# Performance work log

Measured on AMD Instinct MI355X. Metric: run time of the kernel, lower is better.

Reference implementation:

```python
import jax, jax.numpy as jnp
import numpy as np

NC = 80
NA = 3
BOX_GAIN, CLS_GAIN, OBJ_GAIN = 7.5, 0.5, 1.0
GAMMA = 1.5
LS = 0.0
EPS = 1e-7
ANCHORS = np.array([[[10, 13], [16, 30], [33, 23]],
                    [[30, 61], [62, 45], [59, 119]],
                    [[116, 90], [156, 198], [373, 326]]], dtype=np.float32)


def bce_logits(x, t):
    # numerically stable BCE-with-logits, elementwise
    return jnp.maximum(x, 0.0) - x * t + jnp.log1p(jnp.exp(-jnp.abs(x)))


def iou_cxcywh(b1, b2, eps=EPS):
    b1x1, b1x2 = b1[..., 0] - b1[..., 2] / 2, b1[..., 0] + b1[..., 2] / 2
    b1y1, b1y2 = b1[..., 1] - b1[..., 3] / 2, b1[..., 1] + b1[..., 3] / 2
    b2x1, b2x2 = b2[..., 0] - b2[..., 2] / 2, b2[..., 0] + b2[..., 2] / 2
    b2y1, b2y2 = b2[..., 1] - b2[..., 3] / 2, b2[..., 1] + b2[..., 3] / 2
    inter = jnp.clip(jnp.minimum(b1x2, b2x2) - jnp.maximum(b1x1, b2x1), 0.0) * \
            jnp.clip(jnp.minimum(b1y2, b2y2) - jnp.maximum(b1y1, b2y1), 0.0)
    w1, h1 = b1x2 - b1x1, b1y2 - b1y1 + eps
    w2, h2 = b2x2 - b2x1, b2y2 - b2y1 + eps
    union = w1 * h1 + w2 * h2 - inter + eps
    return inter / union


def _scale_loss(pred, targets, anchors):
    B, C, h, w = pred.shape
    p = pred.reshape(B, NA, NC + 5, h, w).transpose(0, 1, 3, 4, 2)  # [B,3,h,w,nc+5]
    pobj = p[..., 4]

    N = targets.shape[0]
    scale = jnp.array([w, h, w, h], dtype=pred.dtype)
    g = targets[:, 2:6] * scale  # grid-space cx,cy,w,h
    gx, gy = g[:, 0], g[:, 1]
    valid = (gx >= 0) & (gx < w) & (gy >= 0) & (gy < h)
    gi = jnp.clip(jnp.floor(gx).astype(jnp.int32), 0, w - 1)
    gj = jnp.clip(jnp.floor(gy).astype(jnp.int32), 0, h - 1)
    bidx = jnp.clip(targets[:, 0].astype(jnp.int32), 0, B - 1)
    cls = jnp.clip(targets[:, 1].astype(jnp.int32), 0, NC - 1)

    # each GT is assigned to all 3 anchors -> M = 3N rows
    rep = lambda v: jnp.repeat(v, NA, axis=0)
    bM, giM, gjM, clsM, maskM = rep(bidx), rep(gi), rep(gj), rep(cls), rep(valid)
    aiM = jnp.tile(jnp.arange(NA), N)
    anchM = anchors[aiM]                             # [M,2]
    txyM = rep(g[:, :2] - jnp.floor(g[:, :2]))       # cell-relative offsets
    twhM = rep(g[:, 2:4])
    mf = maskM.astype(pred.dtype)
    n_valid = mf.sum()

    # objectness target grid (duplicates collapse to 1 via max, like repeated set)
    tobj = jnp.zeros((B, NA, h, w), pred.dtype).at[bM, aiM, gjM, giM].max(mf)
    loss_obj = bce_logits(pobj, tobj).mean() * OBJ_GAIN

    ps = p[bM, aiM, gjM, giM]                        # [M, nc+5]
    ps_box, ps_cls = ps[:, :4], ps[:, 5:]

    # focal classification loss
    t = jax.nn.one_hot(clsM, NC, dtype=pred.dtype)
    if LS > 0:
        t = t * (1 - LS) + LS / NC
    ce = bce_logits(ps_cls, t)
    focal = (1.0 - jnp.exp(-ce)) ** GAMMA * ce       # [M, nc]
    row_sum = (focal * mf[:, None]).sum(-1)          # [M]
    loss_cls = jnp.where(n_valid > 0,
                         row_sum.sum() / (jnp.maximum(n_valid, 1.0) * NC),
                         0.0) * CLS_GAIN

    # per-class focal means (rows grouped by GT class)
    seg_ids = jnp.where(maskM, clsM, NC)
    seg_sum = jax.ops.segment_sum(row_sum, seg_ids, num_segments=NC + 1)[:NC]
    seg_cnt = jax.ops.segment_sum(mf, seg_ids, num_segments=NC + 1)[:NC]
    per_class = jnp.where(seg_cnt > 0,
                          seg_sum / (jnp.maximum(seg_cnt, 1.0) * NC),
                          0.0) * CLS_GAIN

    # box (IoU) loss
    pxy = jax.nn.sigmoid(ps_box[:, :2]) * 2.0 - 0.5
    pwh = (jax.nn.sigmoid(ps_box[:, 2:4]) * 2.0) ** 2 * anchM
    pbox = jnp.concatenate([pxy, pwh], axis=-1)
    tbox = jnp.concatenate([txyM, twhM], axis=-1)
    iou = iou_cxcywh(pbox, tbox)
    loss_box = jnp.where(n_valid > 0,
                         ((1.0 - iou) * mf).sum() / jnp.maximum(n_valid, 1.0),
                         0.0) * BOX_GAIN

    return loss_box, loss_cls, loss_obj, per_class


def setup_inputs() -> dict:
    key = jax.random.key(0)
    k0, k1, k2, kb, kc, kxy, kwh = jax.random.split(key, 7)
    B, N = 16, 800
    p0 = jax.random.normal(k0, (B, NA * (NC + 5), 80, 80), jnp.float32)
    p1 = jax.random.normal(k1, (B, NA * (NC + 5), 40, 40), jnp.float32)
    p2 = jax.random.normal(k2, (B, NA * (NC + 5), 20, 20), jnp.float32)
    bcol = jax.random.randint(kb, (N, 1), 0, B).astype(jnp.float32)
    ccol = jax.random.randint(kc, (N, 1), 0, NC).astype(jnp.float32)
    xy = jax.random.uniform(kxy, (N, 2), jnp.float32, 0.02, 0.98)
    wh = jax.random.uniform(kwh, (N, 2), jnp.float32, 0.02, 0.30)
    targets = jnp.concatenate([bcol, ccol, xy, wh], axis=1)  # [N,6]
    return {"p0": p0, "p1": p1, "p2": p2, "targets": targets}


def reference(p0, p1, p2, targets):
    anchors = jnp.asarray(ANCHORS)
    lb = lc = lo = 0.0
    pc = jnp.zeros((NC,), jnp.float32)
    for i, pred in enumerate((p0, p1, p2)):
        b, c, o, per_class = _scale_loss(pred, targets, anchors[i])
        lb, lc, lo = lb + b, lc + c, lo + o
        pc = pc + per_class
    total = lb + lc + lo
    # [loss, loss_box, loss_cls, loss_obj, per-class cls losses...]
    return jnp.concatenate([jnp.stack([total, lb, lc, lo]), pc])
```

## Files before the change

### kernel.cpp

```cpp
#include <hip/hip_runtime.h>
#include <math.h>

#define NC 80
#define TCOLS 6
#define RPB 15

__device__ __constant__ float c_anch[3][3][2] = {
  {{10.f,13.f},{16.f,30.f},{33.f,23.f}},
  {{30.f,61.f},{62.f,45.f},{59.f,119.f}},
  {{116.f,90.f},{156.f,198.f},{373.f,326.f}}
};

#define ACC_CORR   0
#define ACC_OBJ    16
#define ACC_BOX(s) (32 + 16*(s))
#define ACC_CLS(s) (80 + 16*(s))
#define ACC_NV(s)  (128 + 16*(s))
#define ACC_SEG    176
#define ACC_TOTAL  (176 + 6*NC)

__device__ __forceinline__ float fbce0(float x) {
  return fmaxf(x, 0.f) + __logf(1.f + __expf(-fabsf(x)));
}
__device__ __forceinline__ float fbce(float x, float t) {
  return fmaxf(x, 0.f) - x * t + __logf(1.f + __expf(-fabsf(x)));
}
__device__ __forceinline__ float ffocal(float x, float t) {
  float ce = fbce(x, t);
  float u  = 1.f - __expf(-ce);
  return u * __builtin_amdgcn_sqrtf(u) * ce;
}

__global__ void k_init(float* __restrict__ acc) {
  for (int k = threadIdx.x; k < ACC_TOTAL; k += 256) acc[k] = 0.f;
}

__global__ __launch_bounds__(1024, 8)
void k_fused(const float* __restrict__ p0, const float* __restrict__ p1,
             const float* __restrict__ p2, const float* __restrict__ tgt,
             int N, int B, int RB, int OBJB, float* __restrict__ acc) {
  const int bid = blockIdx.x;
  const int tid = threadIdx.x;
  __shared__ float red[16];

  if (bid < RB) {
    __shared__ float l_box[3], l_cls[3], l_nv[3];
    if (tid < 3) { l_box[tid]=0.f; l_cls[tid]=0.f; l_nv[tid]=0.f; }
    __syncthreads();
    int wv    = tid >> 6;
    int lane  = tid & 63;
    int row   = bid * RPB + wv;
    int nrows = 9 * N;
    if (wv < RPB && row < nrows) {
      int rps = N * 3;
      int s   = row / rps;
      int rem = row - s * rps;
      int n   = rem / 3;
      int a   = rem - n * 3;
      int w   = (s == 0) ? 80 : ((s == 1) ? 40 : 20);
      int hw  = w * w;
      const float* pred = (s == 0) ? p0 : ((s == 1) ? p1 : p2);
      float fw = (float)w;
      float gx = tgt[n*TCOLS + 2] * fw, gy = tgt[n*TCOLS + 3] * fw;
      if (gx >= 0.f && gx < fw && gy >= 0.f && gy < fw) {
        float gw = tgt[n*TCOLS + 4] * fw, gh = tgt[n*TCOLS + 5] * fw;
        int gi  = min(max((int)floorf(gx), 0), w - 1);
        int gj  = min(max((int)floorf(gy), 0), w - 1);
        int b   = min(max((int)tgt[n*TCOLS + 0], 0), B - 1);
        int cls = min(max((int)tgt[n*TCOLS + 1], 0), NC - 1);
        size_t base = (size_t)(b*255 + a*85) * hw + (size_t)(gj*w + gi);

        float x0  = pred[base + (size_t)(5 + lane) * hw];
        float x1  = (lane < 16) ? pred[base + (size_t)(69 + lane) * hw] : 0.f;
        float bxv = (lane < 4)  ? pred[base + (size_t)lane * hw] : 0.f;

        float rs = ffocal(x0, (lane == cls) ? 1.f : 0.f);
        if (lane < 16) rs += ffocal(x1, ((64 + lane) == cls) ? 1.f : 0.f);
        for (int off = 32; off > 0; off >>= 1) rs += __shfl_xor(rs, off, 64);

        float bx = __shfl(bxv, 0, 64), by = __shfl(bxv, 1, 64);
        float bw = __shfl(bxv, 2, 64), bh = __shfl(bxv, 3, 64);
        if (lane == 0) {
          float sx = 1.f/(1.f + __expf(-bx));
          float sy = 1.f/(1.f + __expf(-by));
          float sw = 1.f/(1.f + __expf(-bw));
          float sh = 1.f/(1.f + __expf(-bh));
          float px = sx*2.f - 0.5f, py = sy*2.f - 0.5f;
          float aw = c_anch[s][a][0], ah = c_anch[s][a][1];
          float pw = (sw*2.f)*(sw*2.f)*aw, ph = (sh*2.f)*(sh*2.f)*ah;
          float txf = gx - floorf(gx), tyf = gy - floorf(gy);
          float b1x1 = px - pw*0.5f, b1x2 = px + pw*0.5f;
          float b1y1 = py - ph*0.5f, b1y2 = py + ph*0.5f;
          float b2x1 = txf - gw*0.5f, b2x2 = txf + gw*0.5f;
          float b2y1 = tyf - gh*0.5f, b2y2 = tyf + gh*0.5f;
          float iw = fmaxf(fminf(b1x2, b2x2) - fmaxf(b1x1, b2x1), 0.f);
          float ih = fmaxf(fminf(b1y2, b2y2) - fmaxf(b1y1, b2y1), 0.f);
          float inter = iw * ih;
          float w1 = b1x2 - b1x1, h1 = b1y2 - b1y1 + 1e-7f;
          float w2 = b2x2 - b2x1, h2 = b2y2 - b2y1 + 1e-7f;
          float uni = w1*h1 + w2*h2 - inter + 1e-7f;
          float iou = inter / uni;

          atomicAdd(&l_box[s], 1.f - iou);
          atomicAdd(&l_cls[s], rs);
          atomicAdd(&l_nv[s],  1.f);
          atomicAdd(&acc[ACC_SEG +        s*NC + cls], rs);
          atomicAdd(&acc[ACC_SEG + 3*NC + s*NC + cls], 1.f);
        }
      }
    }
    __syncthreads();
    if (tid < 3) {
      int s = tid; float v;
      v = l_box[s]; if (v != 0.f) atomicAdd(&acc[ACC_BOX(s)], v);
      v = l_cls[s]; if (v != 0.f) atomicAdd(&acc[ACC_CLS(s)], v);
      v = l_nv [s]; if (v != 0.f) atomicAdd(&acc[ACC_NV (s)], v);
    }
  } else if (bid < RB + B) {
    const int bimg = bid - RB;
    __shared__ unsigned cmask[264];
    for (int k = tid; k < 264; k += 1024) cmask[k] = 0u;
    __syncthreads();
    float corr = 0.f;
    for (int n = tid; n < N; n += 1024) {
      int b = min(max((int)tgt[n*TCOLS + 0], 0), B - 1);
      if (b != bimg) continue;
      float tx = tgt[n*TCOLS + 2], ty = tgt[n*TCOLS + 3];
      #pragma unroll
      for (int s = 0; s < 3; ++s) {
        int w  = (s == 0) ? 80 : ((s == 1) ? 40 : 20);
        int hw = w * w;
        float fw = (float)w;
        float gx = tx * fw, gy = ty * fw;
        if (!(gx >= 0.f && gx < fw && gy >= 0.f && gy < fw)) continue;
        int gi = min(max((int)floorf(gx), 0), w - 1);
        int gj = min(max((int)floorf(gy), 0), w - 1);
        int cell = gj * w + gi;
        int bit  = ((s == 0) ? 0 : ((s == 1) ? 6400 : 8000)) + cell;
        unsigned m = 1u << (bit & 31);
        unsigned old = atomicOr(&cmask[bit >> 5], m);
        if (!(old & m)) {
          const float* pred = (s == 0) ? p0 : ((s == 1) ? p1 : p2);
          float inv = 1.f / (float)(B * 3 * hw);
          float sum = pred[(size_t)(bimg*255 +   4) * hw + cell]
                    + pred[(size_t)(bimg*255 +  89) * hw + cell]
                    + pred[(size_t)(bimg*255 + 174) * hw + cell];
          corr -= sum * inv;
        }
      }
    }
    for (int off = 32; off > 0; off >>= 1) corr += __shfl_xor(corr, off, 64);
    if ((tid & 63) == 0) red[tid >> 6] = corr;
    __syncthreads();
    if (tid == 0) {
      float t = 0.f;
      for (int k = 0; k < 16; ++k) t += red[k];
      if (t != 0.f) atomicAdd(&acc[ACC_CORR], t);
    }
  } else {
    const int ob = bid - RB - B;
    const int n0 = B*3*6400, n1 = B*3*1600, n2 = B*3*400;
    const int total4 = (n0 + n1 + n2) >> 2;
    const float i0 = 1.f/(float)n0, i1 = 1.f/(float)n1, i2 = 1.f/(float)n2;
    float local = 0.f;
    for (int i = ob * 1024 + tid; i < total4; i += OBJB * 1024) {
      int e = i << 2;
      const float* pred; int idx, hw; float inv;
      if (e < n0)         { pred = p0; idx = e;           hw = 6400; inv = i0; }
      else if (e < n0+n1) { pred = p1; idx = e - n0;      hw = 1600; inv = i1; }
      else                { pred = p2; idx = e - n0 - n1; hw = 400;  inv = i2; }
      int ba = idx / hw, pix = idx - ba * hw;
      int b = ba / 3, a = ba - b * 3;
      const float4 x4 = *(const float4*)&pred[(size_t)(b*255 + a*85 + 4) * hw + pix];
      local += (fbce0(x4.x) + fbce0(x4.y) + fbce0(x4.z) + fbce0(x4.w)) * inv;
    }
    for (int off = 32; off > 0; off >>= 1) local += __shfl_xor(local, off, 64);
    if ((tid & 63) == 0) red[tid >> 6] = local;
    __syncthreads();
    if (tid == 0) {
      float t = 0.f;
      for (int k = 0; k < 16; ++k) t += red[k];
      atomicAdd(&acc[ACC_OBJ], t);
    }
  }
}

__global__ void k_final(const float* __restrict__ acc, float* __restrict__ out) {
  int t = threadIdx.x;
  if (t == 0) {
    float lo = acc[ACC_OBJ] + acc[ACC_CORR];
    float lb = 0.f, lc = 0.f;
    for (int s = 0; s < 3; ++s) {
      float nv  = acc[ACC_NV(s)];
      float nvm = fmaxf(nv, 1.f);
      if (nv > 0.f) {
        lb += acc[ACC_BOX(s)] / nvm * 7.5f;
        lc += acc[ACC_CLS(s)] / (nvm * (float)NC) * 0.5f;
      }
    }
    out[0] = lb + lc + lo;
    out[1] = lb;
    out[2] = lc;
    out[3] = lo;
  }
  if (t < NC) {
    float pc = 0.f;
    for (int s = 0; s < 3; ++s) {
      float cnt = acc[ACC_SEG + 3*NC + s*NC + t];
      if (cnt > 0.f)
        pc += acc[ACC_SEG + s*NC + t] / (fmaxf(cnt, 1.f) * (float)NC) * 0.5f;
    }
    out[4 + t] = pc;
  }
}

extern "C" void kernel_launch(void* const* d_in, const int* in_sizes, int n_in,
                              void* d_out, int out_size, void* d_ws, size_t ws_size,
                              hipStream_t stream) {
  const float* p0  = (const float*)d_in[0];
  const float* p1  = (const float*)d_in[1];
  const float* p2  = (const float*)d_in[2];
  const float* tgt = (const float*)d_in[3];
  int N = in_sizes[3] / TCOLS;
  int B = in_sizes[0] / (255 * 6400);
  float* out = (float*)d_out;
  float* acc = (float*)d_ws;

  int nrows = 9 * N;
  int RB   = (nrows + RPB - 1) / RPB;
  int OBJB = 512 - RB - B;
  if (OBJB < 1) OBJB = 1;
  int grid = RB + B + OBJB;

  k_init <<<1, 256, 0, stream>>>(acc);
  k_fused<<<grid, 1024, 0, stream>>>(p0, p1, p2, tgt, N, B, RB, OBJB, acc);
  k_final<<<1, 128, 0, stream>>>(acc, out);
}
```

Measured before the change: 35.71 us.

## Fold objectness pass into row blocks' idle wave and use per-block slots

The dedicated objectness blocks are removed. The 16th wave of each row block, previously idle, now handles a contiguous chunk of the objectness BCE sum. Global float atomics for the scalar accumulators are replaced by per-block partial slots in the workspace, which the final kernel reduces. This cuts the grid size and contention on shared atomics, but the objectness stream now runs on only one wave per block.

```diff
diff --git a/kernel.cpp b/kernel.cpp
--- a/kernel.cpp
+++ b/kernel.cpp
@@ -11,13 +11,8 @@
   {{116.f,90.f},{156.f,198.f},{373.f,326.f}}
 };
 
-#define ACC_CORR   0
-#define ACC_OBJ    16
-#define ACC_BOX(s) (32 + 16*(s))
-#define ACC_CLS(s) (80 + 16*(s))
-#define ACC_NV(s)  (128 + 16*(s))
-#define ACC_SEG    176
-#define ACC_TOTAL  (176 + 6*NC)
+#define SEGOFF  0
+#define SLOTOFF 512
 
 __device__ __forceinline__ float fbce0(float x) {
   return fmaxf(x, 0.f) + __logf(1.f + __expf(-fabsf(x)));
@@ -31,94 +26,119 @@
   return u * __builtin_amdgcn_sqrtf(u) * ce;
 }
 
-__global__ void k_init(float* __restrict__ acc) {
-  for (int k = threadIdx.x; k < ACC_TOTAL; k += 256) acc[k] = 0.f;
+__global__ void k_init(float* __restrict__ ws) {
+  for (int k = threadIdx.x; k < 6*NC; k += 256) ws[SEGOFF + k] = 0.f;
 }
 
 __global__ __launch_bounds__(1024, 8)
 void k_fused(const float* __restrict__ p0, const float* __restrict__ p1,
              const float* __restrict__ p2, const float* __restrict__ tgt,
-             int N, int B, int RB, int OBJB, float* __restrict__ acc) {
+             int N, int B, int RB, float* __restrict__ ws) {
   const int bid = blockIdx.x;
   const int tid = threadIdx.x;
-  __shared__ float red[16];
+  float* slot = ws + SLOTOFF + bid * 16;
+  float* seg  = ws + SEGOFF;
 
   if (bid < RB) {
-    __shared__ float l_box[3], l_cls[3], l_nv[3];
+    __shared__ float l_box[3], l_cls[3], l_nv[3], s_obj;
     if (tid < 3) { l_box[tid]=0.f; l_cls[tid]=0.f; l_nv[tid]=0.f; }
     __syncthreads();
-    int wv    = tid >> 6;
-    int lane  = tid & 63;
-    int row   = bid * RPB + wv;
-    int nrows = 9 * N;
-    if (wv < RPB && row < nrows) {
-      int rps = N * 3;
-      int s   = row / rps;
-      int rem = row - s * rps;
-      int n   = rem / 3;
-      int a   = rem - n * 3;
-      int w   = (s == 0) ? 80 : ((s == 1) ? 40 : 20);
-      int hw  = w * w;
-      const float* pred = (s == 0) ? p0 : ((s == 1) ? p1 : p2);
-      float fw = (float)w;
-      float gx = tgt[n*TCOLS + 2] * fw, gy = tgt[n*TCOLS + 3] * fw;
-      if (gx >= 0.f && gx < fw && gy >= 0.f && gy < fw) {
-        float gw = tgt[n*TCOLS + 4] * fw, gh = tgt[n*TCOLS + 5] * fw;
-        int gi  = min(max((int)floorf(gx), 0), w - 1);
-        int gj  = min(max((int)floorf(gy), 0), w - 1);
-        int b   = min(max((int)tgt[n*TCOLS + 0], 0), B - 1);
-        int cls = min(max((int)tgt[n*TCOLS + 1], 0), NC - 1);
-        size_t base = (size_t)(b*255 + a*85) * hw + (size_t)(gj*w + gi);
-
-        float x0  = pred[base + (size_t)(5 + lane) * hw];
-        float x1  = (lane < 16) ? pred[base + (size_t)(69 + lane) * hw] : 0.f;
-        float bxv = (lane < 4)  ? pred[base + (size_t)lane * hw] : 0.f;
-
-        float rs = ffocal(x0, (lane == cls) ? 1.f : 0.f);
-        if (lane < 16) rs += ffocal(x1, ((64 + lane) == cls) ? 1.f : 0.f);
-        for (int off = 32; off > 0; off >>= 1) rs += __shfl_xor(rs, off, 64);
-
-        float bx = __shfl(bxv, 0, 64), by = __shfl(bxv, 1, 64);
-        float bw = __shfl(bxv, 2, 64), bh = __shfl(bxv, 3, 64);
-        if (lane == 0) {
-          float sx = 1.f/(1.f + __expf(-bx));
-          float sy = 1.f/(1.f + __expf(-by));
-          float sw = 1.f/(1.f + __expf(-bw));
-          float sh = 1.f/(1.f + __expf(-bh));
-          float px = sx*2.f - 0.5f, py = sy*2.f - 0.5f;
-          float aw = c_anch[s][a][0], ah = c_anch[s][a][1];
-          float pw = (sw*2.f)*(sw*2.f)*aw, ph = (sh*2.f)*(sh*2.f)*ah;
-          float txf = gx - floorf(gx), tyf = gy - floorf(gy);
-          float b1x1 = px - pw*0.5f, b1x2 = px + pw*0.5f;
-          float b1y1 = py - ph*0.5f, b1y2 = py + ph*0.5f;
-          float b2x1 = txf - gw*0.5f, b2x2 = txf + gw*0.5f;
-          float b2y1 = tyf - gh*0.5f, b2y2 = tyf + gh*0.5f;
-          float iw = fmaxf(fminf(b1x2, b2x2) - fmaxf(b1x1, b2x1), 0.f);
-          float ih = fmaxf(fminf(b1y2, b2y2) - fmaxf(b1y1, b2y1), 0.f);
-          float inter = iw * ih;
-          float w1 = b1x2 - b1x1, h1 = b1y2 - b1y1 + 1e-7f;
-          float w2 = b2x2 - b2x1, h2 = b2y2 - b2y1 + 1e-7f;
-          float uni = w1*h1 + w2*h2 - inter + 1e-7f;
-          float iou = inter / uni;
-
-          atomicAdd(&l_box[s], 1.f - iou);
-          atomicAdd(&l_cls[s], rs);
-          atomicAdd(&l_nv[s],  1.f);
-          atomicAdd(&acc[ACC_SEG +        s*NC + cls], rs);
-          atomicAdd(&acc[ACC_SEG + 3*NC + s*NC + cls], 1.f);
+    int wv   = tid >> 6;
+    int lane = tid & 63;
+    if (wv < RPB) {
+      int row   = bid * RPB + wv;
+      int nrows = 9 * N;
+      if (row < nrows) {
+        int rps = N * 3;
+        int s   = row / rps;
+        int rem = row - s * rps;
+        int n   = rem / 3;
+        int a   = rem - n * 3;
+        int w   = (s == 0) ? 80 : ((s == 1) ? 40 : 20);
+        int hw  = w * w;
+        const float* pred = (s == 0) ? p0 : ((s == 1) ? p1 : p2);
+        float fw = (float)w;
+        float gx = tgt[n*TCOLS + 2] * fw, gy = tgt[n*TCOLS + 3] * fw;
+        if (gx >= 0.f && gx < fw && gy >= 0.f && gy < fw) {
+          float gw = tgt[n*TCOLS + 4] * fw, gh = tgt[n*TCOLS + 5] * fw;
+          int gi  = min(max((int)floorf(gx), 0), w - 1);
+          int gj  = min(max((int)floorf(gy), 0), w - 1);
+          int b   = min(max((int)tgt[n*TCOLS + 0], 0), B - 1);
+          int cls = min(max((int)tgt[n*TCOLS + 1], 0), NC - 1);
+          size_t base = (size_t)(b*255 + a*85) * hw + (size_t)(gj*w + gi);
+
+          float x0  = pred[base + (size_t)(5 + lane) * hw];
+          float x1  = (lane < 16) ? pred[base + (size_t)(69 + lane) * hw] : 0.f;
+          float bxv = (lane < 4)  ? pred[base + (size_t)lane * hw] : 0.f;
+
+          float rs = ffocal(x0, (lane == cls) ? 1.f : 0.f);
+          if (lane < 16) rs += ffocal(x1, ((64 + lane) == cls) ? 1.f : 0.f);
+          for (int off = 32; off > 0; off >>= 1) rs += __shfl_xor(rs, off, 64);
+
+          float bx = __shfl(bxv, 0, 64), by = __shfl(bxv, 1, 64);
+          float bw = __shfl(bxv, 2, 64), bh = __shfl(bxv, 3, 64);
+          if (lane == 0) {
+            float sx = 1.f/(1.f + __expf(-bx));
+            float sy = 1.f/(1.f + __expf(-by));
+            float sw = 1.f/(1.f + __expf(-bw));
+            float sh = 1.f/(1.f + __expf(-bh));
+            float px = sx*2.f - 0.5f, py = sy*2.f - 0.5f;
+            float aw = c_anch[s][a][0], ah = c_anch[s][a][1];
+            float pw = (sw*2.f)*(sw*2.f)*aw, ph = (sh*2.f)*(sh*2.f)*ah;
+            float txf = gx - floorf(gx), tyf = gy - floorf(gy);
+            float b1x1 = px - pw*0.5f, b1x2 = px + pw*0.5f;
+            float b1y1 = py - ph*0.5f, b1y2 = py + ph*0.5f;
+            float b2x1 = txf - gw*0.5f, b2x2 = txf + gw*0.5f;
+            float b2y1 = tyf - gh*0.5f, b2y2 = tyf + gh*0.5f;
+            float iw = fmaxf(fminf(b1x2, b2x2) - fmaxf(b1x1, b2x1), 0.f);
+            float ih = fmaxf(fminf(b1y2, b2y2) - fmaxf(b1y1, b2y1), 0.f);
+            float inter = iw * ih;
+            float w1 = b1x2 - b1x1, h1 = b1y2 - b1y1 + 1e-7f;
+            float w2 = b2x2 - b2x1, h2 = b2y2 - b2y1 + 1e-7f;
+            float uni = w1*h1 + w2*h2 - inter + 1e-7f;
+            float iou = inter / uni;
+
+            atomicAdd(&l_box[s], 1.f - iou);
+            atomicAdd(&l_cls[s], rs);
+            atomicAdd(&l_nv[s],  1.f);
+            atomicAdd(&seg[       s*NC + cls], rs);
+            atomicAdd(&seg[3*NC + s*NC + cls], 1.f);
+          }
         }
       }
+    } else {
+      const int n0 = B*3*6400, n1 = B*3*1600, n2 = B*3*400;
+      const int total4 = (n0 + n1 + n2) >> 2;
+      const int opb = (total4 + RB - 1) / RB;
+      const float i0 = 1.f/(float)n0, i1 = 1.f/(float)n1, i2 = 1.f/(float)n2;
+      int start = bid * opb;
+      int end   = min(start + opb, total4);
+      float local = 0.f;
+      for (int i = start + lane; i < end; i += 64) {
+        int e = i << 2;
+        const float* pred; int idx, hw; float inv;
+        if (e < n0)         { pred = p0; idx = e;           hw = 6400; inv = i0; }
+        else if (e < n0+n1) { pred = p1; idx = e - n0;      hw = 1600; inv = i1; }
+        else                { pred = p2; idx = e - n0 - n1; hw = 400;  inv = i2; }
+        int ba = idx / hw, pix = idx - ba * hw;
+        int b = ba / 3, a = ba - b * 3;
+        const float4 x4 = *(const float4*)&pred[(size_t)(b*255 + a*85 + 4) * hw + pix];
+        local += (fbce0(x4.x) + fbce0(x4.y) + fbce0(x4.z) + fbce0(x4.w)) * inv;
+      }
+      for (int off = 32; off > 0; off >>= 1) local += __shfl_xor(local, off, 64);
+      if (lane == 0) s_obj = local;
     }
     __syncthreads();
     if (tid < 3) {
-      int s = tid; float v;
-      v = l_box[s]; if (v != 0.f) atomicAdd(&acc[ACC_BOX(s)], v);
-      v = l_cls[s]; if (v != 0.f) atomicAdd(&acc[ACC_CLS(s)], v);
-      v = l_nv [s]; if (v != 0.f) atomicAdd(&acc[ACC_NV (s)], v);
-    }
-  } else if (bid < RB + B) {
+      slot[tid    ] = l_box[tid];
+      slot[tid + 3] = l_cls[tid];
+      slot[tid + 6] = l_nv[tid];
+    }
+    if (tid == 0) { slot[9] = s_obj; slot[10] = 0.f; }
+  } else {
     const int bimg = bid - RB;
     __shared__ unsigned cmask[264];
+    __shared__ float red[16];
     for (int k = tid; k < 264; k += 1024) cmask[k] = 0u;
     __syncthreads();
     float corr = 0.f;
@@ -152,50 +172,54 @@
     for (int off = 32; off > 0; off >>= 1) corr += __shfl_xor(corr, off, 64);
     if ((tid & 63) == 0) red[tid >> 6] = corr;
     __syncthreads();
+    if (tid < 10) slot[tid] = 0.f;
     if (tid == 0) {
       float t = 0.f;
       for (int k = 0; k < 16; ++k) t += red[k];
-      if (t != 0.f) atomicAdd(&acc[ACC_CORR], t);
-    }
-  } else {
-    const int ob = bid - RB - B;
-    const int n0 = B*3*6400, n1 = B*3*1600, n2 = B*3*400;
-    const int total4 = (n0 + n1 + n2) >> 2;
-    const float i0 = 1.f/(float)n0, i1 = 1.f/(float)n1, i2 = 1.f/(float)n2;
-    float local = 0.f;
-    for (int i = ob * 1024 + tid; i < total4; i += OBJB * 1024) {
-      int e = i << 2;
-      const float* pred; int idx, hw; float inv;
-      if (e < n0)         { pred = p0; idx = e;           hw = 6400; inv = i0; }
-      else if (e < n0+n1) { pred = p1; idx = e - n0;      hw = 1600; inv = i1; }
-      else                { pred = p2; idx = e - n0 - n1; hw = 400;  inv = i2; }
-      int ba = idx / hw, pix = idx - ba * hw;
-      int b = ba / 3, a = ba - b * 3;
-      const float4 x4 = *(const float4*)&pred[(size_t)(b*255 + a*85 + 4) * hw + pix];
-      local += (fbce0(x4.x) + fbce0(x4.y) + fbce0(x4.z) + fbce0(x4.w)) * inv;
-    }
-    for (int off = 32; off > 0; off >>= 1) local += __shfl_xor(local, off, 64);
-    if ((tid & 63) == 0) red[tid >> 6] = local;
-    __syncthreads();
-    if (tid == 0) {
-      float t = 0.f;
-      for (int k = 0; k < 16; ++k) t += red[k];
-      atomicAdd(&acc[ACC_OBJ], t);
-    }
-  }
-}
-
-__global__ void k_final(const float* __restrict__ acc, float* __restrict__ out) {
-  int t = threadIdx.x;
-  if (t == 0) {
-    float lo = acc[ACC_OBJ] + acc[ACC_CORR];
+      slot[10] = t;
+    }
+  }
+}
+
+__global__ __launch_bounds__(512)
+void k_final(const float* __restrict__ ws, int nblk, float* __restrict__ out) {
+  __shared__ float red[8][11];
+  __shared__ float sS[11];
+  const int tid  = threadIdx.x;
+  const int lane = tid & 63;
+  const int wv   = tid >> 6;
+
+  float v[11];
+  #pragma unroll
+  for (int j = 0; j < 11; ++j) v[j] = 0.f;
+  for (int b = tid; b < nblk; b += 512) {
+    const float* slot = ws + SLOTOFF + b * 16;
+    #pragma unroll
+    for (int j = 0; j < 11; ++j) v[j] += slot[j];
+  }
+  #pragma unroll
+  for (int j = 0; j < 11; ++j)
+    for (int off = 32; off > 0; off >>= 1) v[j] += __shfl_xor(v[j], off, 64);
+  if (lane == 0)
+    #pragma unroll
+    for (int j = 0; j < 11; ++j) red[wv][j] = v[j];
+  __syncthreads();
+  if (tid < 11) {
+    float t = 0.f;
+    for (int k = 0; k < 8; ++k) t += red[k][tid];
+    sS[tid] = t;
+  }
+  __syncthreads();
+
+  if (tid == 0) {
+    float lo = sS[9] + sS[10];
     float lb = 0.f, lc = 0.f;
     for (int s = 0; s < 3; ++s) {
-      float nv  = acc[ACC_NV(s)];
+      float nv  = sS[6 + s];
       float nvm = fmaxf(nv, 1.f);
       if (nv > 0.f) {
-        lb += acc[ACC_BOX(s)] / nvm * 7.5f;
-        lc += acc[ACC_CLS(s)] / (nvm * (float)NC) * 0.5f;
+        lb += sS[s]     / nvm * 7.5f;
+        lc += sS[3 + s] / (nvm * (float)NC) * 0.5f;
       }
     }
     out[0] = lb + lc + lo;
@@ -203,14 +227,14 @@
     out[2] = lc;
     out[3] = lo;
   }
-  if (t < NC) {
+  if (tid < NC) {
     float pc = 0.f;
     for (int s = 0; s < 3; ++s) {
-      float cnt = acc[ACC_SEG + 3*NC + s*NC + t];
+      float cnt = ws[SEGOFF + 3*NC + s*NC + tid];
       if (cnt > 0.f)
-        pc += acc[ACC_SEG + s*NC + t] / (fmaxf(cnt, 1.f) * (float)NC) * 0.5f;
-    }
-    out[4 + t] = pc;
+        pc += ws[SEGOFF + s*NC + tid] / (fmaxf(cnt, 1.f) * (float)NC) * 0.5f;
+    }
+    out[4 + tid] = pc;
   }
 }
 
@@ -224,15 +248,13 @@
   int N = in_sizes[3] / TCOLS;
   int B = in_sizes[0] / (255 * 6400);
   float* out = (float*)d_out;
-  float* acc = (float*)d_ws;
+  float* ws  = (float*)d_ws;
 
   int nrows = 9 * N;
   int RB   = (nrows + RPB - 1) / RPB;
-  int OBJB = 512 - RB - B;
-  if (OBJB < 1) OBJB = 1;
-  int grid = RB + B + OBJB;
-
-  k_init <<<1, 256, 0, stream>>>(acc);
-  k_fused<<<grid, 1024, 0, stream>>>(p0, p1, p2, tgt, N, B, RB, OBJB, acc);
-  k_final<<<1, 128, 0, stream>>>(acc, out);
-}
+  int grid = RB + B;
+
+  k_init <<<1, 256, 0, stream>>>(ws);
+  k_fused<<<grid, 1024, 0, stream>>>(p0, p1, p2, tgt, N, B, RB, ws);
+  k_final<<<1, 512, 0, stream>>>(ws, grid, out);
+}
```

After: 36.57 us. +2.4%, slower.

## Replace per-row class gathers with a coalesced channel stream and split row kernel

Applied to the files above, without the earlier changes.

The old per-target-row gather over 80 class channels is replaced. A streaming kernel now walks every pixel column in float4 chunks, marks which cells hold targets in a shared bitmask, and for those cells sums the zero-target focal loss over all class channels. The per-row sums are scattered to workspace, and a separate row kernel adds the single positive-class correction plus the box IoU. Objectness and duplicate-cell correction are fused into the same stream with per-block slots reduced in the final kernel, which also removes the init kernel. The risk is that the class-channel loads sit outside the mask test and may be issued for every pixel, which would read the whole prediction tensor instead of a sparse subset.

```diff
diff --git a/kernel.cpp b/kernel.cpp
--- a/kernel.cpp
+++ b/kernel.cpp
@@ -3,7 +3,6 @@
 
 #define NC 80
 #define TCOLS 6
-#define RPB 15
 
 __device__ __constant__ float c_anch[3][3][2] = {
   {{10.f,13.f},{16.f,30.f},{33.f,23.f}},
@@ -11,184 +10,264 @@
   {{116.f,90.f},{156.f,198.f},{373.f,326.f}}
 };
 
-#define ACC_CORR   0
-#define ACC_OBJ    16
-#define ACC_BOX(s) (32 + 16*(s))
-#define ACC_CLS(s) (80 + 16*(s))
-#define ACC_NV(s)  (128 + 16*(s))
-#define ACC_SEG    176
-#define ACC_TOTAL  (176 + 6*NC)
+#define ACC_BOX(s) (0  + 16*(s))
+#define ACC_CLS(s) (48 + 16*(s))
+#define ACC_NV(s)  (96 + 16*(s))
+#define ACC_SEG    144
+#define ACC_TOTAL  (144 + 6*NC)
+
+#define S0OFF   1024
+#define SLOTOFF 8704
 
 __device__ __forceinline__ float fbce0(float x) {
   return fmaxf(x, 0.f) + __logf(1.f + __expf(-fabsf(x)));
 }
-__device__ __forceinline__ float fbce(float x, float t) {
-  return fmaxf(x, 0.f) - x * t + __logf(1.f + __expf(-fabsf(x)));
-}
-__device__ __forceinline__ float ffocal(float x, float t) {
-  float ce = fbce(x, t);
-  float u  = 1.f - __expf(-ce);
+__device__ __forceinline__ float fbce1(float x) {
+  return fmaxf(x, 0.f) - x + __logf(1.f + __expf(-fabsf(x)));
+}
+__device__ __forceinline__ float ffoc(float ce) {
+  float u = 1.f - __expf(-ce);
   return u * __builtin_amdgcn_sqrtf(u) * ce;
 }
 
-__global__ void k_init(float* __restrict__ acc) {
-  for (int k = threadIdx.x; k < ACC_TOTAL; k += 256) acc[k] = 0.f;
-}
-
-__global__ __launch_bounds__(1024, 8)
-void k_fused(const float* __restrict__ p0, const float* __restrict__ p1,
-             const float* __restrict__ p2, const float* __restrict__ tgt,
-             int N, int B, int RB, int OBJB, float* __restrict__ acc) {
-  const int bid = blockIdx.x;
+__global__ __launch_bounds__(256)
+void k_stream(const float* __restrict__ p0, const float* __restrict__ p1,
+              const float* __restrict__ p2, const float* __restrict__ tgt,
+              int N, int B, float* __restrict__ ws) {
   const int tid = threadIdx.x;
-  __shared__ float red[16];
-
-  if (bid < RB) {
-    __shared__ float l_box[3], l_cls[3], l_nv[3];
-    if (tid < 3) { l_box[tid]=0.f; l_cls[tid]=0.f; l_nv[tid]=0.f; }
-    __syncthreads();
-    int wv    = tid >> 6;
-    int lane  = tid & 63;
-    int row   = bid * RPB + wv;
-    int nrows = 9 * N;
-    if (wv < RPB && row < nrows) {
-      int rps = N * 3;
-      int s   = row / rps;
-      int rem = row - s * rps;
-      int n   = rem / 3;
-      int a   = rem - n * 3;
-      int w   = (s == 0) ? 80 : ((s == 1) ? 40 : 20);
-      int hw  = w * w;
-      const float* pred = (s == 0) ? p0 : ((s == 1) ? p1 : p2);
+  const int c0  = blockIdx.x * 128;
+  float* acc   = ws;
+  float* s0row = ws + S0OFF;
+  float* slot  = ws + SLOTOFF + blockIdx.x * 16;
+
+  const int b4_1 = B*3*1600;
+  const int b4_2 = b4_1 + B*3*400;
+  const int tot4 = b4_2 + B*3*100;
+
+  __shared__ unsigned umask[16];
+  __shared__ int   pairs[1600];
+  __shared__ int   paircnt;
+  __shared__ float s0lds[512];
+  __shared__ float robj[4], rcorr[4];
+
+  if (tid < 16) umask[tid] = 0u;
+  if (tid == 0) paircnt = 0;
+  if (blockIdx.x == 0)
+    for (int k = tid; k < ACC_TOTAL; k += 256) acc[k] = 0.f;
+  __syncthreads();
+
+  for (int n = tid; n < N; n += 256) {
+    int   b  = min(max((int)tgt[n*TCOLS+0], 0), B-1);
+    float tx = tgt[n*TCOLS+2], ty = tgt[n*TCOLS+3];
+    int base4 = 0;
+    #pragma unroll
+    for (int s = 0; s < 3; ++s) {
+      int w  = (s==0)?80:((s==1)?40:20);
+      int hw = w*w, pc4 = hw>>2;
       float fw = (float)w;
-      float gx = tgt[n*TCOLS + 2] * fw, gy = tgt[n*TCOLS + 3] * fw;
+      float gx = tx*fw, gy = ty*fw;
       if (gx >= 0.f && gx < fw && gy >= 0.f && gy < fw) {
-        float gw = tgt[n*TCOLS + 4] * fw, gh = tgt[n*TCOLS + 5] * fw;
-        int gi  = min(max((int)floorf(gx), 0), w - 1);
-        int gj  = min(max((int)floorf(gy), 0), w - 1);
-        int b   = min(max((int)tgt[n*TCOLS + 0], 0), B - 1);
-        int cls = min(max((int)tgt[n*TCOLS + 1], 0), NC - 1);
-        size_t base = (size_t)(b*255 + a*85) * hw + (size_t)(gj*w + gi);
-
-        float x0  = pred[base + (size_t)(5 + lane) * hw];
-        float x1  = (lane < 16) ? pred[base + (size_t)(69 + lane) * hw] : 0.f;
-        float bxv = (lane < 4)  ? pred[base + (size_t)lane * hw] : 0.f;
-
-        float rs = ffocal(x0, (lane == cls) ? 1.f : 0.f);
-        if (lane < 16) rs += ffocal(x1, ((64 + lane) == cls) ? 1.f : 0.f);
-        for (int off = 32; off > 0; off >>= 1) rs += __shfl_xor(rs, off, 64);
-
-        float bx = __shfl(bxv, 0, 64), by = __shfl(bxv, 1, 64);
-        float bw = __shfl(bxv, 2, 64), bh = __shfl(bxv, 3, 64);
-        if (lane == 0) {
-          float sx = 1.f/(1.f + __expf(-bx));
-          float sy = 1.f/(1.f + __expf(-by));
-          float sw = 1.f/(1.f + __expf(-bw));
-          float sh = 1.f/(1.f + __expf(-bh));
-          float px = sx*2.f - 0.5f, py = sy*2.f - 0.5f;
-          float aw = c_anch[s][a][0], ah = c_anch[s][a][1];
-          float pw = (sw*2.f)*(sw*2.f)*aw, ph = (sh*2.f)*(sh*2.f)*ah;
-          float txf = gx - floorf(gx), tyf = gy - floorf(gy);
-          float b1x1 = px - pw*0.5f, b1x2 = px + pw*0.5f;
-          float b1y1 = py - ph*0.5f, b1y2 = py + ph*0.5f;
-          float b2x1 = txf - gw*0.5f, b2x2 = txf + gw*0.5f;
-          float b2y1 = tyf - gh*0.5f, b2y2 = tyf + gh*0.5f;
-          float iw = fmaxf(fminf(b1x2, b2x2) - fmaxf(b1x1, b2x1), 0.f);
-          float ih = fmaxf(fminf(b1y2, b2y2) - fmaxf(b1y1, b2y1), 0.f);
-          float inter = iw * ih;
-          float w1 = b1x2 - b1x1, h1 = b1y2 - b1y1 + 1e-7f;
-          float w2 = b2x2 - b2x1, h2 = b2y2 - b2y1 + 1e-7f;
-          float uni = w1*h1 + w2*h2 - inter + 1e-7f;
-          float iou = inter / uni;
-
-          atomicAdd(&l_box[s], 1.f - iou);
-          atomicAdd(&l_cls[s], rs);
-          atomicAdd(&l_nv[s],  1.f);
-          atomicAdd(&acc[ACC_SEG +        s*NC + cls], rs);
-          atomicAdd(&acc[ACC_SEG + 3*NC + s*NC + cls], 1.f);
+        int gi = min(max((int)floorf(gx),0), w-1);
+        int gj = min(max((int)floorf(gy),0), w-1);
+        int cell = gj*w + gi;
+        for (int a = 0; a < 3; ++a) {
+          int col4 = base4 + (b*3+a)*pc4 + (cell>>2);
+          int loc  = col4 - c0;
+          if (loc >= 0 && loc < 128) {
+            int bit = loc*4 + (cell&3);
+            atomicOr(&umask[bit>>5], 1u<<(bit&31));
+            int idx = atomicAdd(&paircnt, 1);
+            if (idx < 1600) pairs[idx] = (bit<<13) | (s*(N*3) + n*3 + a);
+          }
         }
       }
-    }
-    __syncthreads();
-    if (tid < 3) {
-      int s = tid; float v;
-      v = l_box[s]; if (v != 0.f) atomicAdd(&acc[ACC_BOX(s)], v);
-      v = l_cls[s]; if (v != 0.f) atomicAdd(&acc[ACC_CLS(s)], v);
-      v = l_nv [s]; if (v != 0.f) atomicAdd(&acc[ACC_NV (s)], v);
-    }
-  } else if (bid < RB + B) {
-    const int bimg = bid - RB;
-    __shared__ unsigned cmask[264];
-    for (int k = tid; k < 264; k += 1024) cmask[k] = 0u;
-    __syncthreads();
-    float corr = 0.f;
-    for (int n = tid; n < N; n += 1024) {
-      int b = min(max((int)tgt[n*TCOLS + 0], 0), B - 1);
-      if (b != bimg) continue;
-      float tx = tgt[n*TCOLS + 2], ty = tgt[n*TCOLS + 3];
-      #pragma unroll
-      for (int s = 0; s < 3; ++s) {
-        int w  = (s == 0) ? 80 : ((s == 1) ? 40 : 20);
-        int hw = w * w;
-        float fw = (float)w;
-        float gx = tx * fw, gy = ty * fw;
-        if (!(gx >= 0.f && gx < fw && gy >= 0.f && gy < fw)) continue;
-        int gi = min(max((int)floorf(gx), 0), w - 1);
-        int gj = min(max((int)floorf(gy), 0), w - 1);
-        int cell = gj * w + gi;
-        int bit  = ((s == 0) ? 0 : ((s == 1) ? 6400 : 8000)) + cell;
-        unsigned m = 1u << (bit & 31);
-        unsigned old = atomicOr(&cmask[bit >> 5], m);
-        if (!(old & m)) {
-          const float* pred = (s == 0) ? p0 : ((s == 1) ? p1 : p2);
-          float inv = 1.f / (float)(B * 3 * hw);
-          float sum = pred[(size_t)(bimg*255 +   4) * hw + cell]
-                    + pred[(size_t)(bimg*255 +  89) * hw + cell]
-                    + pred[(size_t)(bimg*255 + 174) * hw + cell];
-          corr -= sum * inv;
+      base4 += B*3*pc4;
+    }
+  }
+  __syncthreads();
+
+  const int  col4 = c0 + (tid>>1);
+  const int  half = tid & 1;
+  const int  loc  = col4 - c0;
+  float  obj = 0.f, corr = 0.f;
+  float4 S0  = {0.f, 0.f, 0.f, 0.f};
+  if (col4 < tot4) {
+    int hw, pc4, i;
+    const float* pred;
+    if (col4 < b4_1)      { hw=6400; pc4=1600; i=col4;      pred=p0; }
+    else if (col4 < b4_2) { hw=1600; pc4=400;  i=col4-b4_1; pred=p1; }
+    else                  { hw=400;  pc4=100;  i=col4-b4_2; pred=p2; }
+    int ba  = i / pc4;
+    int pix = (i - ba*pc4) * 4;
+    int b   = ba / 3, a = ba - b*3;
+    float inv = 1.f / (float)(B*3*hw);
+    size_t base = (size_t)(b*255 + a*85)*hw + pix;
+    unsigned m = (umask[loc>>3] >> ((loc&7)*4)) & 0xFu;
+
+    if (half == 0) {
+      float4 xo = *(const float4*)(pred + base + (size_t)4*hw);
+      obj = (fbce0(xo.x)+fbce0(xo.y)+fbce0(xo.z)+fbce0(xo.w)) * inv;
+      if (m) {
+        float cs = 0.f;
+        if (m&1) cs += xo.x;
+        if (m&2) cs += xo.y;
+        if (m&4) cs += xo.z;
+        if (m&8) cs += xo.w;
+        corr = -cs * inv;
+      }
+      #pragma unroll 4
+      for (int ch = 5; ch < 45; ++ch) {
+        float4 x4 = *(const float4*)(pred + base + (size_t)ch*hw);
+        if (m) {
+          if (m&1) S0.x += ffoc(fbce0(x4.x));
+          if (m&2) S0.y += ffoc(fbce0(x4.y));
+          if (m&4) S0.z += ffoc(fbce0(x4.z));
+          if (m&8) S0.w += ffoc(fbce0(x4.w));
         }
       }
-    }
-    for (int off = 32; off > 0; off >>= 1) corr += __shfl_xor(corr, off, 64);
-    if ((tid & 63) == 0) red[tid >> 6] = corr;
-    __syncthreads();
-    if (tid == 0) {
-      float t = 0.f;
-      for (int k = 0; k < 16; ++k) t += red[k];
-      if (t != 0.f) atomicAdd(&acc[ACC_CORR], t);
-    }
-  } else {
-    const int ob = bid - RB - B;
-    const int n0 = B*3*6400, n1 = B*3*1600, n2 = B*3*400;
-    const int total4 = (n0 + n1 + n2) >> 2;
-    const float i0 = 1.f/(float)n0, i1 = 1.f/(float)n1, i2 = 1.f/(float)n2;
-    float local = 0.f;
-    for (int i = ob * 1024 + tid; i < total4; i += OBJB * 1024) {
-      int e = i << 2;
-      const float* pred; int idx, hw; float inv;
-      if (e < n0)         { pred = p0; idx = e;           hw = 6400; inv = i0; }
-      else if (e < n0+n1) { pred = p1; idx = e - n0;      hw = 1600; inv = i1; }
-      else                { pred = p2; idx = e - n0 - n1; hw = 400;  inv = i2; }
-      int ba = idx / hw, pix = idx - ba * hw;
-      int b = ba / 3, a = ba - b * 3;
-      const float4 x4 = *(const float4*)&pred[(size_t)(b*255 + a*85 + 4) * hw + pix];
-      local += (fbce0(x4.x) + fbce0(x4.y) + fbce0(x4.z) + fbce0(x4.w)) * inv;
-    }
-    for (int off = 32; off > 0; off >>= 1) local += __shfl_xor(local, off, 64);
-    if ((tid & 63) == 0) red[tid >> 6] = local;
-    __syncthreads();
-    if (tid == 0) {
-      float t = 0.f;
-      for (int k = 0; k < 16; ++k) t += red[k];
-      atomicAdd(&acc[ACC_OBJ], t);
-    }
-  }
-}
-
-__global__ void k_final(const float* __restrict__ acc, float* __restrict__ out) {
-  int t = threadIdx.x;
-  if (t == 0) {
-    float lo = acc[ACC_OBJ] + acc[ACC_CORR];
+    } else {
+      #pragma unroll 4
+      for (int ch = 45; ch < 85; ++ch) {
+        float4 x4 = *(const float4*)(pred + base + (size_t)ch*hw);
+        if (m) {
+          if (m&1) S0.x += ffoc(fbce0(x4.x));
+          if (m&2) S0.y += ffoc(fbce0(x4.y));
+          if (m&4) S0.z += ffoc(fbce0(x4.z));
+          if (m&8) S0.w += ffoc(fbce0(x4.w));
+        }
+      }
+    }
+  }
+  S0.x += __shfl_xor(S0.x, 1, 64);
+  S0.y += __shfl_xor(S0.y, 1, 64);
+  S0.z += __shfl_xor(S0.z, 1, 64);
+  S0.w += __shfl_xor(S0.w, 1, 64);
+  if (col4 < tot4 && half == 0)
+    *(float4*)&s0lds[loc*4] = S0;
+
+  for (int off = 32; off > 0; off >>= 1) {
+    obj  += __shfl_xor(obj,  off, 64);
+    corr += __shfl_xor(corr, off, 64);
+  }
+  if ((tid & 63) == 0) { robj[tid>>6] = obj; rcorr[tid>>6] = corr; }
+  __syncthreads();
+
+  int pcnt = min(paircnt, 1600);
+  for (int ii = tid; ii < pcnt; ii += 256) {
+    int pk = pairs[ii];
+    s0row[pk & 8191] = s0lds[pk >> 13];
+  }
+  if (tid == 0) {
+    slot[0] = robj[0] + robj[1] + robj[2] + robj[3];
+    slot[1] = rcorr[0] + rcorr[1] + rcorr[2] + rcorr[3];
+  }
+}
+
+__global__ __launch_bounds__(256)
+void k_rows(const float* __restrict__ p0, const float* __restrict__ p1,
+            const float* __restrict__ p2, const float* __restrict__ tgt,
+            int N, int B, float* __restrict__ ws) {
+  __shared__ float l_box[3], l_cls[3], l_nv[3];
+  float* acc   = ws;
+  float* s0row = ws + S0OFF;
+  const int tid = threadIdx.x;
+  if (tid < 3) { l_box[tid]=0.f; l_cls[tid]=0.f; l_nv[tid]=0.f; }
+  __syncthreads();
+
+  int r = blockIdx.x * 256 + tid;
+  int nrows = 9 * N;
+  if (r < nrows) {
+    int s   = r / (3*N);
+    int rem = r - s*3*N;
+    int n   = rem / 3;
+    int a   = rem - n*3;
+    int w   = (s==0)?80:((s==1)?40:20);
+    int hw  = w*w;
+    const float* pred = (s==0)?p0:((s==1)?p1:p2);
+    float fw = (float)w;
+    float gx = tgt[n*TCOLS+2]*fw, gy = tgt[n*TCOLS+3]*fw;
+    if (gx >= 0.f && gx < fw && gy >= 0.f && gy < fw) {
+      float gw = tgt[n*TCOLS+4]*fw, gh = tgt[n*TCOLS+5]*fw;
+      int gi  = min(max((int)floorf(gx),0), w-1);
+      int gj  = min(max((int)floorf(gy),0), w-1);
+      int b   = min(max((int)tgt[n*TCOLS+0], 0), B-1);
+      int cls = min(max((int)tgt[n*TCOLS+1], 0), NC-1);
+      size_t base = (size_t)(b*255 + a*85)*hw + (size_t)(gj*w + gi);
+
+      float bx = pred[base];
+      float by = pred[base + (size_t)hw];
+      float bw = pred[base + 2*(size_t)hw];
+      float bh = pred[base + 3*(size_t)hw];
+      float xr = pred[base + (size_t)(5 + cls)*hw];
+      float s0v = s0row[r];
+
+      float rs = s0v + ffoc(fbce1(xr)) - ffoc(fbce0(xr));
+
+      float sx = 1.f/(1.f + __expf(-bx));
+      float sy = 1.f/(1.f + __expf(-by));
+      float sw = 1.f/(1.f + __expf(-bw));
+      float sh = 1.f/(1.f + __expf(-bh));
+      float px = sx*2.f - 0.5f, py = sy*2.f - 0.5f;
+      float aw = c_anch[s][a][0], ah = c_anch[s][a][1];
+      float pw = (sw*2.f)*(sw*2.f)*aw, ph = (sh*2.f)*(sh*2.f)*ah;
+      float txf = gx - floorf(gx), tyf = gy - floorf(gy);
+      float b1x1 = px - pw*0.5f, b1x2 = px + pw*0.5f;
+      float b1y1 = py - ph*0.5f, b1y2 = py + ph*0.5f;
+      float b2x1 = txf - gw*0.5f, b2x2 = txf + gw*0.5f;
+      float b2y1 = tyf - gh*0.5f, b2y2 = tyf + gh*0.5f;
+      float iw = fmaxf(fminf(b1x2, b2x2) - fmaxf(b1x1, b2x1), 0.f);
+      float ih = fmaxf(fminf(b1y2, b2y2) - fmaxf(b1y1, b2y1), 0.f);
+      float inter = iw * ih;
+      float w1 = b1x2 - b1x1, h1 = b1y2 - b1y1 + 1e-7f;
+      float w2 = b2x2 - b2x1, h2 = b2y2 - b2y1 + 1e-7f;
+      float uni = w1*h1 + w2*h2 - inter + 1e-7f;
+      float iou = inter / uni;
+
+      atomicAdd(&l_box[s], 1.f - iou);
+      atomicAdd(&l_cls[s], rs);
+      atomicAdd(&l_nv[s],  1.f);
+      atomicAdd(&acc[ACC_SEG +        s*NC + cls], rs);
+      atomicAdd(&acc[ACC_SEG + 3*NC + s*NC + cls], 1.f);
+    }
+  }
+  __syncthreads();
+  if (tid < 3) {
+    int s = tid; float v;
+    v = l_box[s]; if (v != 0.f) atomicAdd(&acc[ACC_BOX(s)], v);
+    v = l_cls[s]; if (v != 0.f) atomicAdd(&acc[ACC_CLS(s)], v);
+    v = l_nv [s]; if (v != 0.f) atomicAdd(&acc[ACC_NV (s)], v);
+  }
+}
+
+__global__ __launch_bounds__(512)
+void k_final(const float* __restrict__ ws, int nblk, float* __restrict__ out) {
+  __shared__ float red[8][2];
+  __shared__ float sOC[2];
+  const int tid  = threadIdx.x;
+  const int lane = tid & 63;
+  const int wv   = tid >> 6;
+  const float* acc = ws;
+
+  float v0 = 0.f, v1 = 0.f;
+  for (int b = tid; b < nblk; b += 512) {
+    const float* slot = ws + SLOTOFF + b*16;
+    v0 += slot[0]; v1 += slot[1];
+  }
+  for (int off = 32; off > 0; off >>= 1) {
+    v0 += __shfl_xor(v0, off, 64);
+    v1 += __shfl_xor(v1, off, 64);
+  }
+  if (lane == 0) { red[wv][0] = v0; red[wv][1] = v1; }
+  __syncthreads();
+  if (tid < 2) {
+    float t = 0.f;
+    for (int k = 0; k < 8; ++k) t += red[k][tid];
+    sOC[tid] = t;
+  }
+  __syncthreads();
+
+  if (tid == 0) {
+    float lo = sOC[0] + sOC[1];
     float lb = 0.f, lc = 0.f;
     for (int s = 0; s < 3; ++s) {
       float nv  = acc[ACC_NV(s)];
@@ -203,14 +282,14 @@
     out[2] = lc;
     out[3] = lo;
   }
-  if (t < NC) {
+  if (tid < NC) {
     float pc = 0.f;
     for (int s = 0; s < 3; ++s) {
-      float cnt = acc[ACC_SEG + 3*NC + s*NC + t];
+      float cnt = acc[ACC_SEG + 3*NC + s*NC + tid];
       if (cnt > 0.f)
-        pc += acc[ACC_SEG + s*NC + t] / (fmaxf(cnt, 1.f) * (float)NC) * 0.5f;
-    }
-    out[4 + t] = pc;
+        pc += acc[ACC_SEG + s*NC + tid] / (fmaxf(cnt, 1.f) * (float)NC) * 0.5f;
+    }
+    out[4 + tid] = pc;
   }
 }
 
@@ -224,15 +303,14 @@
   int N = in_sizes[3] / TCOLS;
   int B = in_sizes[0] / (255 * 6400);
   float* out = (float*)d_out;
-  float* acc = (float*)d_ws;
-
-  int nrows = 9 * N;
-  int RB   = (nrows + RPB - 1) / RPB;
-  int OBJB = 512 - RB - B;
-  if (OBJB < 1) OBJB = 1;
-  int grid = RB + B + OBJB;
-
-  k_init <<<1, 256, 0, stream>>>(acc);
-  k_fused<<<grid, 1024, 0, stream>>>(p0, p1, p2, tgt, N, B, RB, OBJB, acc);
-  k_final<<<1, 128, 0, stream>>>(acc, out);
-}
+  float* ws  = (float*)d_ws;
+
+  int tot4   = B * 3 * (1600 + 400 + 100);
+  int nchunk = (tot4 + 127) / 128;
+  int nrows  = 9 * N;
+  int rb     = (nrows + 255) / 256;
+
+  k_stream<<<nchunk, 256, 0, stream>>>(p0, p1, p2, tgt, N, B, ws);
+  k_rows  <<<rb,     256, 0, stream>>>(p0, p1, p2, tgt, N, B, ws);
+  k_final <<<1,      512, 0, stream>>>(ws, nchunk, out);
+}
```

New measurement: 84.74 us. 137% more time.
